# Kernel tuning notes

Hardware: AMD Instinct MI355X
Metric: run time of the kernel (lower is better)

## Reference

```python
import jax, jax.numpy as jnp
import numpy as np

OSF = 15.0  # over_sample_factor
EXPMAX = 50.0
AFROMZERO = 0.02
AFROMC = 0.01


def zmax_calc(a, b, c=1.0):
    # a is a scalar, b (= b*mT^2) is per-element, c == 1.0
    a_is_zero = a < AFROMZERO
    a_is_c = jnp.abs(a - c) < AFROMC
    z_zero = jnp.where(c > b, b / c, 1.0)
    z_c = b / (b + c)
    denom = jnp.where(a_is_c, 1.0, c - a)  # safe denom; branch masked below
    z_gen = 0.5 * (b + c - jnp.sqrt((b - c) ** 2 + 4.0 * a * b)) / denom
    z_gen = jnp.where((z_gen > 0.9999) & (b > 100.0), jnp.minimum(z_gen, 1.0 - a / b), z_gen)
    return jnp.where(a_is_zero, z_zero, jnp.where(a_is_c, z_c, z_gen))


def likelihood(z, mT, a, b):
    # Lund fragmentation f(z) ratio kernel, c = 1.0
    b_exp = b * mT ** 2
    z_max = zmax_calc(a, b_exp, 1.0)
    f_exp = b_exp * (1.0 / z_max - 1.0 / z) + jnp.log(z_max / z)
    a_coef = a * jnp.log((1.0 - z) / (1.0 - z_max))
    f_exp = f_exp + jnp.where(a < AFROMZERO, 0.0, a_coef)
    return jnp.exp(jnp.clip(f_exp, -EXPMAX, EXPMAX))


def setup_inputs() -> dict:
    key = jax.random.key(0)
    kz, kr, km, kmult, kdrop, kzero = jax.random.split(key, 6)
    B, M, R = 8192, 128, 24  # batch, max multiplicity, reject slots
    mult = jax.random.randint(kmult, (B,), 20, M + 1)  # event multiplicities
    valid = jnp.arange(M)[None, :] < mult[:, None]  # [B, M]

    z_acc = jax.random.uniform(kz, (B, M), minval=0.05, maxval=0.95)
    z_acc = jnp.where(valid & (jax.random.uniform(kzero, (B, M)) > 0.1), z_acc, 0.0)

    z_rej = jax.random.uniform(kr, (B, M, R), minval=0.05, maxval=0.95)
    keep = jax.random.uniform(kdrop, (B, M, R)) < 0.4  # ragged # of rejections
    z_rej = jnp.where(valid[:, :, None] & keep, z_rej, 0.0)

    z = jnp.concatenate([z_acc[:, :, None], z_rej], axis=2).astype(jnp.float32)
    mT = jax.random.uniform(km, (B, M), minval=0.2, maxval=2.0, dtype=jnp.float32)
    observable = jnp.stack([mult, jnp.zeros_like(mult)], axis=1).astype(jnp.int64)

    return {
        "z": z,
        "mT": mT,
        "observable": observable,
        "params_a": jnp.float32(0.72),
        "params_b": jnp.float32(1.05),
        "params_base": jnp.array([0.68, 0.98], dtype=jnp.float32),
    }


def reference(z, mT, observable, params_a, params_b, params_base):
    B, M, _ = z.shape
    mult = observable[:, 0]
    valid = jnp.arange(M)[None, :] < mult[:, None]  # [B, M]
    a0, b0 = params_base[0], params_base[1]

    # accepted z's (column 0)
    z_acc = z[:, :, 0]
    m_acc = (z_acc != 0.0) & valid
    zs = jnp.where(m_acc, z_acc, 0.5)  # safe fill for masked slots
    mTs = jnp.where(m_acc, mT, 1.0)
    w_acc = likelihood(zs, mTs, params_a, params_b) / likelihood(zs, mTs, a0, b0)
    w_acc = jnp.where(m_acc, w_acc, 1.0)

    # rejected z's (columns 1:), each row j uses mT[i, j]
    z_rej = z[:, :, 1:]
    m_rej = (z_rej != 0.0) & valid[:, :, None]
    zr = jnp.where(m_rej, z_rej, 0.5)
    mTr = jnp.where(m_rej, mT[:, :, None], 1.0)
    w_rej = (OSF - likelihood(zr, mTr, params_a, params_b)) / (
        OSF - likelihood(zr, mTr, a0, b0))
    w_rej = jnp.where(m_rej, w_rej, 1.0)

    return jnp.prod(w_acc, axis=1) * jnp.prod(w_rej, axis=(1, 2))
```

## Files before the change

kernel.cpp:

```cpp
#include <hip/hip_runtime.h>

#define AFROMZERO 0.02f
#define AFROMC    0.01f
#define OSF       15.0f
#define EXPMAX    50.0f

__device__ __forceinline__ float zmax_calc(float a, float b) {
    if (a < AFROMZERO) {
        return fminf(b, 1.0f);
    }
    if (fabsf(a - 1.0f) < AFROMC) {
        return b / (b + 1.0f);
    }
    float denom = 1.0f - a;
    float d = (b - 1.0f) * (b - 1.0f) + 4.0f * a * b;
    float zg = 0.5f * (b + 1.0f - sqrtf(d)) / denom;
    if (zg > 0.9999f && b > 100.0f) zg = fminf(zg, 1.0f - a / b);
    return zg;
}

__device__ __forceinline__ void set_consts(float a, float b, float mTv,
                                           float& C, float& be) {
    be = b * mTv * mTv;
    float zm  = zmax_calc(a, be);
    float inv = 1.0f / zm;
    float c   = be * inv + logf(zm);
    if (a >= AFROMZERO) c -= a * logf(1.0f - zm);
    C = c;
}

__global__ __launch_bounds__(256) void lund_weight_kernel(
    const float* __restrict__ z,
    const float* __restrict__ mT,
    const int*   __restrict__ obs,
    const float* __restrict__ pa_p,
    const float* __restrict__ pb_p,
    const float* __restrict__ base_p,
    float* __restrict__ out)
{
    const int b   = blockIdx.x;
    const int tid = threadIdx.x;

    const float pa = pa_p[0];
    const float pb = pb_p[0];
    const float a0 = base_p[0];
    const float b0 = base_p[1];
    const float aeff_n = (pa < AFROMZERO) ? 0.0f : pa;
    const float aeff_o = (a0 < AFROMZERO) ? 0.0f : a0;
    const int   mult   = obs[2 * b];

    __shared__ float4 s_p[128];
    __shared__ double s_part[4];

    if (tid < 128) {
        float mTv = mT[(size_t)b * 128 + tid];
        float Cn, ben, Co, beo;
        set_consts(pa, pb, mTv, Cn, ben);
        set_consts(a0, b0, mTv, Co, beo);
        s_p[tid] = make_float4(Cn, ben, Co, beo);
    }
    __syncthreads();

    const float4* zrow = (const float4*)(z + (size_t)b * 3200);
    double prod = 1.0;

    for (int i = tid; i < 800; i += 256) {
        float4 zv = zrow[i];
        int e = 4 * i;
        int m = e / 25;
        int r = e - 25 * m;
        float zza[4] = {zv.x, zv.y, zv.z, zv.w};
        #pragma unroll
        for (int j = 0; j < 4; ++j) {
            float zz = zza[j];
            bool active = (zz != 0.0f) && (m < mult);
            float zs = active ? zz : 0.5f;
            float4 p = s_p[m];

            float rz = __builtin_amdgcn_rcpf(zs);
            float lz = __logf(zs);
            float l1 = __logf(1.0f - zs);

            float fn = fmaf(-p.y, rz, p.x) - lz + aeff_n * l1;
            float fo = fmaf(-p.w, rz, p.z) - lz + aeff_o * l1;
            fn = fminf(fmaxf(fn, -EXPMAX), EXPMAX);
            fo = fminf(fmaxf(fo, -EXPMAX), EXPMAX);
            float Ln = __expf(fn);
            float Lo = __expf(fo);

            float num = (r == 0) ? Ln : (OSF - Ln);
            float den = (r == 0) ? Lo : (OSF - Lo);
            float w = active ? (num * __builtin_amdgcn_rcpf(den)) : 1.0f;
            prod *= (double)w;

            if (++r == 25) { r = 0; ++m; }
        }
    }

    for (int mask = 1; mask < 64; mask <<= 1)
        prod *= __shfl_xor(prod, mask, 64);
    if ((tid & 63) == 0) s_part[tid >> 6] = prod;
    __syncthreads();
    if (tid == 0)
        out[b] = (float)(s_part[0] * s_part[1] * s_part[2] * s_part[3]);
}

extern "C" void kernel_launch(void* const* d_in, const int* in_sizes, int n_in,
                              void* d_out, int out_size, void* d_ws, size_t ws_size,
                              hipStream_t stream) {
    const float* z    = (const float*)d_in[0];
    const float* mT   = (const float*)d_in[1];
    const int*   obs  = (const int*)d_in[2];
    const float* pa   = (const float*)d_in[3];
    const float* pb   = (const float*)d_in[4];
    const float* base = (const float*)d_in[5];
    float* out = (float*)d_out;

    int B = in_sizes[0] / (128 * 25);
    lund_weight_kernel<<<B, 256, 0, stream>>>(z, mT, obs, pa, pb, base, out);
}
```

Before: 174.9 us.

## Stage z rows in LDS, one thread per particle, skip invalid slots

Each block now handles two events. It copies only the valid prefix of each z row (mult*25 floats) into shared memory, and each thread owns one particle. Per thread, the 25 likelihood terms are accumulated as separate numerator and denominator products with a single division at the end. The math moves to base-2 log/exp intrinsics, and double-precision accumulation is replaced by float. This cuts global reads for padded slots, per-element divisions and FP64 multiplies and shuffles, but float products may overflow or lose accuracy, and shared-memory reads with a stride of 25 may cause bank conflicts.

```diff
diff --git a/kernel.cpp b/kernel.cpp
--- a/kernel.cpp
+++ b/kernel.cpp
@@ -3,30 +3,26 @@
 #define AFROMZERO 0.02f
 #define AFROMC    0.01f
 #define OSF       15.0f
-#define EXPMAX    50.0f
+#define LOG2E     1.4426950408889634f
+#define EXPMAX2   (50.0f * LOG2E)
 
 __device__ __forceinline__ float zmax_calc(float a, float b) {
-    if (a < AFROMZERO) {
-        return fminf(b, 1.0f);
-    }
-    if (fabsf(a - 1.0f) < AFROMC) {
-        return b / (b + 1.0f);
-    }
-    float denom = 1.0f - a;
-    float d = (b - 1.0f) * (b - 1.0f) + 4.0f * a * b;
-    float zg = 0.5f * (b + 1.0f - sqrtf(d)) / denom;
+    if (a < AFROMZERO) return fminf(b, 1.0f);
+    if (fabsf(a - 1.0f) < AFROMC) return b / (b + 1.0f);
+    float d  = (b - 1.0f) * (b - 1.0f) + 4.0f * a * b;
+    float zg = 0.5f * (b + 1.0f - sqrtf(d)) / (1.0f - a);
     if (zg > 0.9999f && b > 100.0f) zg = fminf(zg, 1.0f - a / b);
     return zg;
 }
 
-__device__ __forceinline__ void set_consts(float a, float b, float mTv,
-                                           float& C, float& be) {
-    be = b * mTv * mTv;
-    float zm  = zmax_calc(a, be);
-    float inv = 1.0f / zm;
-    float c   = be * inv + logf(zm);
-    if (a >= AFROMZERO) c -= a * logf(1.0f - zm);
-    C = c;
+__device__ __forceinline__ void set_consts2(float a, float b, float mTv,
+                                            float& C2, float& be2) {
+    float be = b * mTv * mTv;
+    float zm = zmax_calc(a, be);
+    be2 = be * LOG2E;
+    float c = be2 / zm + log2f(zm);
+    if (a >= AFROMZERO) c -= a * log2f(1.0f - zm);
+    C2 = c;
 }
 
 __global__ __launch_bounds__(256) void lund_weight_kernel(
@@ -38,71 +34,73 @@
     const float* __restrict__ base_p,
     float* __restrict__ out)
 {
-    const int b   = blockIdx.x;
+    __shared__ float4 s_z4[1600];
+    __shared__ float  s_part[4];
+    float* s_z = (float*)s_z4;
+
     const int tid = threadIdx.x;
+    const int r0  = blockIdx.x * 2;
 
-    const float pa = pa_p[0];
-    const float pb = pb_p[0];
-    const float a0 = base_p[0];
-    const float b0 = base_p[1];
-    const float aeff_n = (pa < AFROMZERO) ? 0.0f : pa;
-    const float aeff_o = (a0 < AFROMZERO) ? 0.0f : a0;
-    const int   mult   = obs[2 * b];
+    const int mult0 = obs[2 * r0];
+    const int mult1 = obs[2 * r0 + 2];
+    const int n4_0 = (mult0 * 25 + 3) >> 2;
+    const int n4_1 = (mult1 * 25 + 3) >> 2;
+    const float4* g = (const float4*)(z + (size_t)r0 * 3200);
+    for (int i = tid; i < 800; i += 256) {
+        if (i < n4_0) s_z4[i]       = g[i];
+        if (i < n4_1) s_z4[800 + i] = g[800 + i];
+    }
 
-    __shared__ float4 s_p[128];
-    __shared__ double s_part[4];
+    const int  half = tid >> 7;
+    const int  m    = tid & 127;
+    const int  row  = r0 + half;
+    const int  mult = half ? mult1 : mult0;
+    const bool live = m < mult;
 
-    if (tid < 128) {
-        float mTv = mT[(size_t)b * 128 + tid];
-        float Cn, ben, Co, beo;
-        set_consts(pa, pb, mTv, Cn, ben);
-        set_consts(a0, b0, mTv, Co, beo);
-        s_p[tid] = make_float4(Cn, ben, Co, beo);
-    }
+    const float pa = pa_p[0], pb = pb_p[0];
+    const float a0 = base_p[0], b0 = base_p[1];
+    const float an = (pa < AFROMZERO) ? 0.0f : pa;
+    const float ao = (a0 < AFROMZERO) ? 0.0f : a0;
+
+    const float mTv = mT[(size_t)row * 128 + m];
+    float Cn2, ben2, Co2, beo2;
+    set_consts2(pa, pb, mTv, Cn2, ben2);
+    set_consts2(a0, b0, mTv, Co2, beo2);
+
     __syncthreads();
 
-    const float4* zrow = (const float4*)(z + (size_t)b * 3200);
-    double prod = 1.0;
-
-    for (int i = tid; i < 800; i += 256) {
-        float4 zv = zrow[i];
-        int e = 4 * i;
-        int m = e / 25;
-        int r = e - 25 * m;
-        float zza[4] = {zv.x, zv.y, zv.z, zv.w};
+    float w = 1.0f;
+    if (live) {
+        const float* zp = s_z + half * 3200 + m * 25;
+        float facN = 1.0f, facD = 1.0f;
         #pragma unroll
-        for (int j = 0; j < 4; ++j) {
-            float zz = zza[j];
-            bool active = (zz != 0.0f) && (m < mult);
-            float zs = active ? zz : 0.5f;
-            float4 p = s_p[m];
-
-            float rz = __builtin_amdgcn_rcpf(zs);
-            float lz = __logf(zs);
-            float l1 = __logf(1.0f - zs);
-
-            float fn = fmaf(-p.y, rz, p.x) - lz + aeff_n * l1;
-            float fo = fmaf(-p.w, rz, p.z) - lz + aeff_o * l1;
-            fn = fminf(fmaxf(fn, -EXPMAX), EXPMAX);
-            fo = fminf(fmaxf(fo, -EXPMAX), EXPMAX);
-            float Ln = __expf(fn);
-            float Lo = __expf(fo);
-
-            float num = (r == 0) ? Ln : (OSF - Ln);
-            float den = (r == 0) ? Lo : (OSF - Lo);
-            float w = active ? (num * __builtin_amdgcn_rcpf(den)) : 1.0f;
-            prod *= (double)w;
-
-            if (++r == 25) { r = 0; ++m; }
+        for (int k = 0; k < 25; ++k) {
+            float zz  = zp[k];
+            bool  act = (zz != 0.0f);
+            float zs  = act ? zz : 0.5f;
+            float rz  = __builtin_amdgcn_rcpf(zs);
+            float lz  = __builtin_amdgcn_logf(zs);
+            float l1  = __builtin_amdgcn_logf(1.0f - zs);
+            float fn  = fmaf(-ben2, rz, Cn2) + fmaf(an, l1, -lz);
+            float fo  = fmaf(-beo2, rz, Co2) + fmaf(ao, l1, -lz);
+            fn = fminf(fmaxf(fn, -EXPMAX2), EXPMAX2);
+            fo = fminf(fmaxf(fo, -EXPMAX2), EXPMAX2);
+            float Ln = __builtin_amdgcn_exp2f(fn);
+            float Lo = __builtin_amdgcn_exp2f(fo);
+            float fN = (k == 0) ? Ln : (OSF - Ln);
+            float fD = (k == 0) ? Lo : (OSF - Lo);
+            facN *= act ? fN : 1.0f;
+            facD *= act ? fD : 1.0f;
         }
+        w = facN / facD;
     }
 
     for (int mask = 1; mask < 64; mask <<= 1)
-        prod *= __shfl_xor(prod, mask, 64);
-    if ((tid & 63) == 0) s_part[tid >> 6] = prod;
+        w *= __shfl_xor(w, mask, 64);
+    if ((tid & 63) == 0) s_part[tid >> 6] = w;
     __syncthreads();
-    if (tid == 0)
-        out[b] = (float)(s_part[0] * s_part[1] * s_part[2] * s_part[3]);
+    if (tid == 0)   out[r0]     = s_part[0] * s_part[1];
+    if (tid == 128) out[r0 + 1] = s_part[2] * s_part[3];
 }
 
 extern "C" void kernel_launch(void* const* d_in, const int* in_sizes, int n_in,
@@ -117,5 +115,5 @@
     float* out = (float*)d_out;
 
     int B = in_sizes[0] / (128 * 25);
-    lund_weight_kernel<<<B, 256, 0, stream>>>(z, mT, obs, pa, pb, base, out);
+    lund_weight_kernel<<<B / 2, 256, 0, stream>>>(z, mT, obs, pa, pb, base, out);
 }
```

After: 163.0 us. -6.8%, faster.
